# Kernel tuning notes

Hardware: AMD Instinct MI355X
Metric: run time of the kernel (lower is better)

The kernel has to match this reference:

```python
import jax, jax.numpy as jnp
import numpy as np

B, S, T, E, H = 2, 2048, 2048, 1024, 16
HD = E // H  # head_dim = 64


def setup_inputs() -> dict:
    key = jax.random.key(0)
    ks = jax.random.split(key, 12)
    sc = 1.0 / np.sqrt(E)
    inp = {
        "query": jax.random.normal(ks[0], (B, S, E), jnp.float32),
        "key": jax.random.normal(ks[1], (B, T, E), jnp.float32),
        "value": jax.random.normal(ks[2], (B, T, E), jnp.float32),
        "attn_mask": jnp.ones((S, T), jnp.int32),
        # nn.Linear params: y = x @ W.T + b
        "Wq": jax.random.normal(ks[3], (E, E), jnp.float32) * sc,
        "bq": jax.random.normal(ks[4], (E,), jnp.float32) * sc,
        "Wk": jax.random.normal(ks[5], (E, E), jnp.float32) * sc,
        "bk": jax.random.normal(ks[6], (E,), jnp.float32) * sc,
        "Wv": jax.random.normal(ks[7], (E, E), jnp.float32) * sc,
        "bv": jax.random.normal(ks[8], (E,), jnp.float32) * sc,
        "Wo": jax.random.normal(ks[9], (E, E), jnp.float32) * sc,
        "bo": jax.random.normal(ks[10], (E,), jnp.float32) * sc,
    }
    return inp


def reference(query, key, value, attn_mask, Wq, bq, Wk, bk, Wv, bv, Wo, bo):
    N, Sq, Ed = query.shape
    Tk = key.shape[1]
    # projections (torch Linear: x @ W.T + b)
    q = query @ Wq.T + bq
    k = key @ Wk.T + bk
    v = value @ Wv.T + bv
    # split heads -> (N, H, S, HD)
    q = q.reshape(N, Sq, H, HD).transpose(0, 2, 1, 3)
    k = k.reshape(N, Tk, H, HD).transpose(0, 2, 1, 3)
    v = v.reshape(N, Tk, H, HD).transpose(0, 2, 1, 3)
    # scaled dot-product scores: (N, H, S, T)
    energy = jnp.einsum("nhsd,nhtd->nhst", q, k) / jnp.sqrt(jnp.float32(HD))
    energy = jnp.where(attn_mask[None, None, :, :] == 0, -jnp.inf, energy)
    attn = jax.nn.softmax(energy, axis=3)
    # dropout is identity in eval mode
    out = jnp.einsum("nhst,nhtd->nshd", attn, v).reshape(N, Sq, Ed)
    return out @ Wo.T + bo
```

## Files before the change

kernel.cpp:

```cpp
#include <hip/hip_runtime.h>

typedef __attribute__((ext_vector_type(8))) short short8;
typedef __attribute__((ext_vector_type(4))) float f32x4;
typedef __attribute__((ext_vector_type(16))) float f32x16;

#define DEV __device__ __forceinline__

constexpr int Bb = 2, Ss = 2048, Tt = 2048, Ee = 1024, Hh = 16, HDd = 64;
constexpr int Mm = Bb * Ss;
constexpr size_t NX = (size_t)Mm * Ee;
constexpr size_t NW = (size_t)Ee * Ee;

constexpr size_t OFF_XQ   = 0;
constexpr size_t OFF_XK   = OFF_XQ + NX * 2;
constexpr size_t OFF_XV   = OFF_XK + NX * 2;
constexpr size_t OFF_WQ   = OFF_XV + NX * 2;
constexpr size_t OFF_WK   = OFF_WQ + NW * 2;
constexpr size_t OFF_WV   = OFF_WK + NW * 2;
constexpr size_t OFF_WO   = OFF_WV + NW * 2;
constexpr size_t OFF_QH   = OFF_WO + NW * 2;
constexpr size_t OFF_KH   = OFF_QH + NX * 2;
constexpr size_t OFF_VH   = OFF_KH + NX * 2;
constexpr size_t OFF_OB   = OFF_VH + NX * 2;
constexpr size_t OFF_FLAG = OFF_OB + NX * 2;

DEV unsigned short f2bf(float f) {
  union { float f; unsigned u; } v; v.f = f;
  unsigned r = v.u + 0x7fffu + ((v.u >> 16) & 1u);
  return (unsigned short)(r >> 16);
}

#define GLDS16(g, l) __builtin_amdgcn_global_load_lds(                         \
    (const __attribute__((address_space(1))) void*)(g),                        \
    (__attribute__((address_space(3))) void*)(l), 16, 0, 0)

#define PLSWAP(a, b) asm("v_permlane32_swap_b32 %0, %1" : "+v"(a), "+v"(b))
#define CVTPK(d, lo, hi_) asm("v_cvt_pk_bf16_f32 %0, %1, %2" : "=v"(d) : "v"(lo), "v"(hi_))

#if __has_builtin(__builtin_amdgcn_exp2f)
#define EXP2(x) __builtin_amdgcn_exp2f(x)
#else
#define EXP2(x) exp2f(x)
#endif

__global__ __launch_bounds__(256) void prep_kernel(
    const float* __restrict__ q, const float* __restrict__ k, const float* __restrict__ v,
    const float* __restrict__ wq, const float* __restrict__ wk,
    const float* __restrict__ wv, const float* __restrict__ wo,
    const int* __restrict__ mask,
    unsigned short* __restrict__ Xq, unsigned short* __restrict__ Xk, unsigned short* __restrict__ Xv,
    unsigned short* __restrict__ Wqb, unsigned short* __restrict__ Wkb,
    unsigned short* __restrict__ Wvb, unsigned short* __restrict__ Wob,
    int* __restrict__ flagZero)
{
  constexpr size_t NXv = NX / 4, NWv = NW / 4;
  constexpr size_t tot = 4 * NXv + 4 * NWv;
  for (size_t u = (size_t)blockIdx.x * blockDim.x + threadIdx.x; u < tot;
       u += (size_t)gridDim.x * blockDim.x) {
    if (u < 3 * NXv) {
      const float* src; unsigned short* dst; size_t off;
      if (u < NXv)            { src = q; dst = Xq; off = u; }
      else if (u < 2 * NXv)   { src = k; dst = Xk; off = u - NXv; }
      else                    { src = v; dst = Xv; off = u - 2 * NXv; }
      float4 f = ((const float4*)src)[off];
      ushort4 o; o.x = f2bf(f.x); o.y = f2bf(f.y); o.z = f2bf(f.z); o.w = f2bf(f.w);
      ((ushort4*)dst)[off] = o;
    } else if (u < 3 * NXv + 4 * NWv) {
      size_t uu = u - 3 * NXv;
      int wsel = (int)(uu / NWv); size_t off = uu % NWv;
      const float* src = wsel == 0 ? wq : wsel == 1 ? wk : wsel == 2 ? wv : wo;
      unsigned short* dst = wsel == 0 ? Wqb : wsel == 1 ? Wkb : wsel == 2 ? Wvb : Wob;
      float4 f = ((const float4*)src)[off];
      ushort4 o; o.x = f2bf(f.x); o.y = f2bf(f.y); o.z = f2bf(f.z); o.w = f2bf(f.w);
      ((ushort4*)dst)[off] = o;
    } else {
      size_t off = u - 3 * NXv - 4 * NWv;
      int4 m = ((const int4*)mask)[off];
      if (m.x == 0 || m.y == 0 || m.z == 0 || m.w == 0) *flagZero = 1;
    }
  }
}

DEV void gemm128(const unsigned short* __restrict__ A, const unsigned short* __restrict__ Bm,
                 unsigned short* Asm, unsigned short* Bsm, f32x4 acc[4][4], int K)
{
  const int t = threadIdx.x;
  const int w = t >> 6, lane = t & 63;
  const int l15 = lane & 15, l4 = lane >> 4;
  const int wm = w >> 1, wn = w & 1;
  const int srow = lane >> 2;
  const int skc  = (lane & 3) * 8;
#pragma unroll
  for (int mi = 0; mi < 4; ++mi)
#pragma unroll
    for (int ni = 0; ni < 4; ++ni) acc[mi][ni] = (f32x4){0.f, 0.f, 0.f, 0.f};

  for (int k0 = 0; k0 < K; k0 += 32) {
    GLDS16(A  + (size_t)(w * 16 + srow) * K + k0 + skc,        Asm + w * 512);
    GLDS16(A  + (size_t)(64 + w * 16 + srow) * K + k0 + skc,   Asm + 2048 + w * 512);
    GLDS16(Bm + (size_t)(w * 16 + srow) * K + k0 + skc,        Bsm + w * 512);
    GLDS16(Bm + (size_t)(64 + w * 16 + srow) * K + k0 + skc,   Bsm + 2048 + w * 512);
    __syncthreads();
    short8 af[4], bf[4];
#pragma unroll
    for (int mi = 0; mi < 4; ++mi)
      af[mi] = *(const short8*)&Asm[(wm * 64 + mi * 16 + l15) * 32 + l4 * 8];
#pragma unroll
    for (int ni = 0; ni < 4; ++ni)
      bf[ni] = *(const short8*)&Bsm[(wn * 64 + ni * 16 + l15) * 32 + l4 * 8];
#pragma unroll
    for (int mi = 0; mi < 4; ++mi)
#pragma unroll
      for (int ni = 0; ni < 4; ++ni)
        acc[mi][ni] = __builtin_amdgcn_mfma_f32_16x16x32_bf16(af[mi], bf[ni], acc[mi][ni], 0, 0, 0);
    __syncthreads();
  }
}

__global__ __launch_bounds__(256) void gemm_qkv(
    const unsigned short* __restrict__ Xq, const unsigned short* __restrict__ Xk,
    const unsigned short* __restrict__ Xv,
    const unsigned short* __restrict__ Wqb, const unsigned short* __restrict__ Wkb,
    const unsigned short* __restrict__ Wvb,
    const float* __restrict__ bq, const float* __restrict__ bk, const float* __restrict__ bv,
    unsigned short* __restrict__ Qh, unsigned short* __restrict__ Kh, unsigned short* __restrict__ Vh)
{
  __shared__ unsigned short Asm[128 * 32], Bsm[128 * 32];
  const int z = blockIdx.z;
  const unsigned short* A  = (z == 0) ? Xq  : (z == 1) ? Xk  : Xv;
  const unsigned short* Bw = (z == 0) ? Wqb : (z == 1) ? Wkb : Wvb;
  const float* bias        = (z == 0) ? bq  : (z == 1) ? bk  : bv;
  unsigned short* Out      = (z == 0) ? Qh  : (z == 1) ? Kh  : Vh;
  const int by = blockIdx.y, bx = blockIdx.x;
  f32x4 acc[4][4];
  gemm128(A + (size_t)by * 128 * Ee, Bw + (size_t)bx * 128 * Ee, Asm, Bsm, acc, Ee);
  const int t = threadIdx.x, w = t >> 6, lane = t & 63, l15 = lane & 15, l4 = lane >> 4;
  const int wm = w >> 1, wn = w & 1;
#pragma unroll
  for (int ni = 0; ni < 4; ++ni) {
    int col = bx * 128 + wn * 64 + ni * 16 + l15;
    float bcol = bias[col];
    int h = col >> 6, hd = col & 63;
#pragma unroll
    for (int mi = 0; mi < 4; ++mi) {
#pragma unroll
      for (int r = 0; r < 4; ++r) {
        int row = by * 128 + wm * 64 + mi * 16 + l4 * 4 + r;
        int b = row >> 11, s = row & 2047;
        Out[(((size_t)(b * Hh + h)) * Ss + s) * HDd + hd] = f2bf(acc[mi][ni][r] + bcol);
      }
    }
  }
}

__global__ __launch_bounds__(256) void gemm_out(
    const unsigned short* __restrict__ Ob, const unsigned short* __restrict__ Wob,
    const float* __restrict__ bo, float* __restrict__ out)
{
  __shared__ unsigned short Asm[128 * 32], Bsm[128 * 32];
  const int by = blockIdx.y, bx = blockIdx.x;
  f32x4 acc[4][4];
  gemm128(Ob + (size_t)by * 128 * Ee, Wob + (size_t)bx * 128 * Ee, Asm, Bsm, acc, Ee);
  const int t = threadIdx.x, w = t >> 6, lane = t & 63, l15 = lane & 15, l4 = lane >> 4;
  const int wm = w >> 1, wn = w & 1;
#pragma unroll
  for (int ni = 0; ni < 4; ++ni) {
    int col = bx * 128 + wn * 64 + ni * 16 + l15;
    float bcol = bo[col];
#pragma unroll
    for (int mi = 0; mi < 4; ++mi) {
#pragma unroll
      for (int r = 0; r < 4; ++r) {
        int row = by * 128 + wm * 64 + mi * 16 + l4 * 4 + r;
        out[(size_t)row * Ee + col] = acc[mi][ni][r] + bcol;
      }
    }
  }
}

__global__ __launch_bounds__(256) void attn_kernel(
    const unsigned short* __restrict__ Qh, const unsigned short* __restrict__ Kh,
    const unsigned short* __restrict__ Vh, const int* __restrict__ mask,
    const int* __restrict__ flagZero, unsigned short* __restrict__ Ob)
{
  __shared__ unsigned short Ks[2][64 * 64];
  __shared__ unsigned short Vt[2][64 * 72];
  const int bh = blockIdx.y, qt = blockIdx.x;
  const int tid = threadIdx.x, w = tid >> 6, lane = tid & 63;
  const int l31 = lane & 31, hi = lane >> 5;
  const bool useMask = (*flagZero != 0);
  const size_t bhBase = (size_t)bh * Ss * HDd;
  const int s0 = qt * 128 + w * 32;
  const float SCL = 0.18033688f;

  short8 qf[4];
#pragma unroll
  for (int ks = 0; ks < 4; ++ks)
    qf[ks] = *(const short8*)&Qh[bhBase + (size_t)(s0 + l31) * 64 + ks * 16 + hi * 8];

  f32x16 o0, o1;
#pragma unroll
  for (int r = 0; r < 16; ++r) { o0[r] = 0.f; o1[r] = 0.f; }
  float m_r = -1e30f, l_r = 0.f;

  const int kc0 = tid, kc1 = tid + 256;
  const int kr0 = kc0 >> 3, kg0 = (kc0 & 7) ^ (kr0 & 7);
  const int kr1 = kc1 >> 3, kg1 = (kc1 & 7) ^ (kr1 & 7);

  GLDS16(Kh + bhBase + (size_t)kr0 * 64 + kg0 * 8, &Ks[0][0] + w * 512);
  GLDS16(Kh + bhBase + (size_t)kr1 * 64 + kg1 * 8, &Ks[0][0] + 2048 + w * 512);
  {
    const unsigned short* vs = Vh + bhBase + (size_t)lane * 64 + w * 16;
    short8 v0 = *(const short8*)vs, v1 = *(const short8*)(vs + 8);
#pragma unroll
    for (int k2 = 0; k2 < 8; ++k2) Vt[0][(w * 16 + k2) * 72 + lane] = (unsigned short)v0[k2];
#pragma unroll
    for (int k2 = 0; k2 < 8; ++k2) Vt[0][(w * 16 + 8 + k2) * 72 + lane] = (unsigned short)v1[k2];
  }
  __syncthreads();

  int cur = 0;
  for (int kt = 0; kt < Tt; kt += 64) {
    const bool last = (kt + 64 >= Tt);
    short8 v0, v1;
    if (!last) {
      GLDS16(Kh + bhBase + (size_t)(kt + 64 + kr0) * 64 + kg0 * 8, &Ks[cur ^ 1][0] + w * 512);
      GLDS16(Kh + bhBase + (size_t)(kt + 64 + kr1) * 64 + kg1 * 8, &Ks[cur ^ 1][0] + 2048 + w * 512);
      const unsigned short* vs = Vh + bhBase + (size_t)(kt + 64 + lane) * 64 + w * 16;
      v0 = *(const short8*)vs; v1 = *(const short8*)(vs + 8);
    }

    f32x16 p0, p1;
#pragma unroll
    for (int r = 0; r < 16; ++r) { p0[r] = 0.f; p1[r] = 0.f; }
    const unsigned short* Kc = &Ks[cur][0];
#pragma unroll
    for (int ks = 0; ks < 4; ++ks) {
      int row0 = l31, row1 = 32 + l31;
      short8 ka0 = *(const short8*)&Kc[row0 * 64 + (((ks * 2 + hi) ^ (row0 & 7)) * 8)];
      short8 ka1 = *(const short8*)&Kc[row1 * 64 + (((ks * 2 + hi) ^ (row1 & 7)) * 8)];
      p0 = __builtin_amdgcn_mfma_f32_32x32x16_bf16(ka0, qf[ks], p0, 0, 0, 0);
      p1 = __builtin_amdgcn_mfma_f32_32x32x16_bf16(ka1, qf[ks], p1, 0, 0, 0);
    }

    if (useMask) {
      int sg = s0 + l31;
#pragma unroll
      for (int r = 0; r < 16; ++r) {
        int tg = kt + (r & 3) + 8 * (r >> 2) + 4 * hi;
        if (mask[(size_t)sg * Tt + tg] == 0)      p0[r] = -1e30f;
        if (mask[(size_t)sg * Tt + tg + 32] == 0) p1[r] = -1e30f;
      }
    }

    float pmax = p0[0];
#pragma unroll
    for (int r = 1; r < 16; ++r) pmax = fmaxf(pmax, p0[r]);
#pragma unroll
    for (int r = 0; r < 16; ++r) pmax = fmaxf(pmax, p1[r]);
    pmax = fmaxf(pmax, __shfl_xor(pmax, 32));

    if (!__all(pmax - m_r <= 44.0f)) {
      float mnew = fmaxf(m_r, pmax);
      float alpha = EXP2((m_r - mnew) * SCL);
      l_r *= alpha;
#pragma unroll
      for (int r = 0; r < 16; ++r) {
        int sr = (r & 3) + 8 * (r >> 2) + 4 * hi;
        float ar = __shfl(alpha, sr);
        o0[r] *= ar; o1[r] *= ar;
      }
      m_r = mnew;
    }
    float mm = m_r * SCL;
    float ps = 0.f;
#pragma unroll
    for (int r = 0; r < 16; ++r) { p0[r] = EXP2(fmaf(p0[r], SCL, -mm)); ps += p0[r]; }
#pragma unroll
    for (int r = 0; r < 16; ++r) { p1[r] = EXP2(fmaf(p1[r], SCL, -mm)); ps += p1[r]; }
    l_r += ps + __shfl_xor(ps, 32);

    short8 pa[4];
#define PACKKS(ks, PV)                                                         \
    {                                                                          \
      unsigned a0, a1, b0, b1; const int bse = 8 * ((ks) & 1);                 \
      CVTPK(a0, PV[bse + 0], PV[bse + 1]);                                     \
      CVTPK(a1, PV[bse + 2], PV[bse + 3]);                                     \
      CVTPK(b0, PV[bse + 4], PV[bse + 5]);                                     \
      CVTPK(b1, PV[bse + 6], PV[bse + 7]);                                     \
      PLSWAP(a0, b0); PLSWAP(a1, b1);                                          \
      union { unsigned u[4]; short8 s; } cc;                                   \
      cc.u[0] = a0; cc.u[1] = a1; cc.u[2] = b0; cc.u[3] = b1;                  \
      pa[ks] = cc.s;                                                           \
    }
    PACKKS(0, p0) PACKKS(1, p0) PACKKS(2, p1) PACKKS(3, p1)
#undef PACKKS

    const unsigned short* Vc = &Vt[cur][0];
#pragma unroll
    for (int ks = 0; ks < 4; ++ks) {
      short8 vf0 = *(const short8*)&Vc[(l31) * 72 + ks * 16 + hi * 8];
      short8 vf1 = *(const short8*)&Vc[(32 + l31) * 72 + ks * 16 + hi * 8];
      o0 = __builtin_amdgcn_mfma_f32_32x32x16_bf16(pa[ks], vf0, o0, 0, 0, 0);
      o1 = __builtin_amdgcn_mfma_f32_32x32x16_bf16(pa[ks], vf1, o1, 0, 0, 0);
    }

    if (!last) {
#pragma unroll
      for (int k2 = 0; k2 < 8; ++k2) Vt[cur ^ 1][(w * 16 + k2) * 72 + lane] = (unsigned short)v0[k2];
#pragma unroll
      for (int k2 = 0; k2 < 8; ++k2) Vt[cur ^ 1][(w * 16 + 8 + k2) * 72 + lane] = (unsigned short)v1[k2];
    }
    __syncthreads();
    cur ^= 1;
  }

  const int b = bh >> 4, h = bh & 15;
  float linv = l_r > 0.f ? 1.0f / l_r : 0.f;
#pragma unroll
  for (int r = 0; r < 16; ++r) {
    int sr = (r & 3) + 8 * (r >> 2) + 4 * hi;
    float li = __shfl(linv, sr);
    size_t rowbase = (size_t)(b * Ss + s0 + sr) * Ee + h * 64;
    Ob[rowbase + l31]      = f2bf(o0[r] * li);
    Ob[rowbase + 32 + l31] = f2bf(o1[r] * li);
  }
}

extern "C" void kernel_launch(void* const* d_in, const int* in_sizes, int n_in,
                              void* d_out, int out_size, void* d_ws, size_t ws_size,
                              hipStream_t stream) {
  const float* q   = (const float*)d_in[0];
  const float* k   = (const float*)d_in[1];
  const float* v   = (const float*)d_in[2];
  const int*  msk  = (const int*)d_in[3];
  const float* Wq  = (const float*)d_in[4];
  const float* bq  = (const float*)d_in[5];
  const float* Wk  = (const float*)d_in[6];
  const float* bk  = (const float*)d_in[7];
  const float* Wv  = (const float*)d_in[8];
  const float* bv  = (const float*)d_in[9];
  const float* Wo  = (const float*)d_in[10];
  const float* bo  = (const float*)d_in[11];
  float* out = (float*)d_out;

  char* ws = (char*)d_ws;
  unsigned short* Xq  = (unsigned short*)(ws + OFF_XQ);
  unsigned short* Xk  = (unsigned short*)(ws + OFF_XK);
  unsigned short* Xv  = (unsigned short*)(ws + OFF_XV);
  unsigned short* Wqb = (unsigned short*)(ws + OFF_WQ);
  unsigned short* Wkb = (unsigned short*)(ws + OFF_WK);
  unsigned short* Wvb = (unsigned short*)(ws + OFF_WV);
  unsigned short* Wob = (unsigned short*)(ws + OFF_WO);
  unsigned short* Qh  = (unsigned short*)(ws + OFF_QH);
  unsigned short* Kh  = (unsigned short*)(ws + OFF_KH);
  unsigned short* Vh  = (unsigned short*)(ws + OFF_VH);
  unsigned short* Ob  = (unsigned short*)(ws + OFF_OB);
  int* flagZero       = (int*)(ws + OFF_FLAG);

  hipMemsetAsync(flagZero, 0, 4, stream);
  prep_kernel<<<4096, 256, 0, stream>>>(q, k, v, Wq, Wk, Wv, Wo, msk,
                                        Xq, Xk, Xv, Wqb, Wkb, Wvb, Wob, flagZero);
  gemm_qkv<<<dim3(8, 32, 3), 256, 0, stream>>>(Xq, Xk, Xv, Wqb, Wkb, Wvb,
                                               bq, bk, bv, Qh, Kh, Vh);
  attn_kernel<<<dim3(16, 32), 256, 0, stream>>>(Qh, Kh, Vh, msk, flagZero, Ob);
  gemm_out<<<dim3(8, 32), 256, 0, stream>>>(Ob, Wob, bo, out);
}
```

Measured before the change: 151.6 us.

## Split attention KV range across wave pairs and merge partial softmax in LDS

Each block now covers 64 query rows instead of 128, and two waves share each 32-row group while handling alternate 64-key tiles of every 128-key chunk. The partial (m, l, O) states are merged through shared memory at the end. The grid doubles to 1024 blocks with a launch-bounds occupancy hint, and setprio is placed around the MFMA sections. The max and sum reductions are also rewritten as trees. In exchange, the software double-buffered prefetch is dropped: loads now happen synchronously each iteration with two barriers, which may expose memory latency, and the final merge adds LDS traffic.

```diff
diff --git a/kernel.cpp b/kernel.cpp
--- a/kernel.cpp
+++ b/kernel.cpp
@@ -178,7 +178,7 @@
   }
 }
 
-__global__ __launch_bounds__(256) void attn_kernel(
+__global__ __launch_bounds__(256, 4) void attn_kernel(
     const unsigned short* __restrict__ Qh, const unsigned short* __restrict__ Kh,
     const unsigned short* __restrict__ Vh, const int* __restrict__ mask,
     const int* __restrict__ flagZero, unsigned short* __restrict__ Ob)
@@ -188,9 +188,10 @@
   const int bh = blockIdx.y, qt = blockIdx.x;
   const int tid = threadIdx.x, w = tid >> 6, lane = tid & 63;
   const int l31 = lane & 31, hi = lane >> 5;
+  const int g = w >> 1, p = w & 1;
   const bool useMask = (*flagZero != 0);
   const size_t bhBase = (size_t)bh * Ss * HDd;
-  const int s0 = qt * 128 + w * 32;
+  const int s0 = qt * 64 + g * 32;
   const float SCL = 0.18033688f;
 
   short8 qf[4];
@@ -203,37 +204,36 @@
   for (int r = 0; r < 16; ++r) { o0[r] = 0.f; o1[r] = 0.f; }
   float m_r = -1e30f, l_r = 0.f;
 
-  const int kc0 = tid, kc1 = tid + 256;
-  const int kr0 = kc0 >> 3, kg0 = (kc0 & 7) ^ (kr0 & 7);
-  const int kr1 = kc1 >> 3, kg1 = (kc1 & 7) ^ (kr1 & 7);
-
-  GLDS16(Kh + bhBase + (size_t)kr0 * 64 + kg0 * 8, &Ks[0][0] + w * 512);
-  GLDS16(Kh + bhBase + (size_t)kr1 * 64 + kg1 * 8, &Ks[0][0] + 2048 + w * 512);
-  {
-    const unsigned short* vs = Vh + bhBase + (size_t)lane * 64 + w * 16;
-    short8 v0 = *(const short8*)vs, v1 = *(const short8*)(vs + 8);
-#pragma unroll
-    for (int k2 = 0; k2 < 8; ++k2) Vt[0][(w * 16 + k2) * 72 + lane] = (unsigned short)v0[k2];
-#pragma unroll
-    for (int k2 = 0; k2 < 8; ++k2) Vt[0][(w * 16 + 8 + k2) * 72 + lane] = (unsigned short)v1[k2];
-  }
-  __syncthreads();
-
-  int cur = 0;
-  for (int kt = 0; kt < Tt; kt += 64) {
-    const bool last = (kt + 64 >= Tt);
-    short8 v0, v1;
-    if (!last) {
-      GLDS16(Kh + bhBase + (size_t)(kt + 64 + kr0) * 64 + kg0 * 8, &Ks[cur ^ 1][0] + w * 512);
-      GLDS16(Kh + bhBase + (size_t)(kt + 64 + kr1) * 64 + kg1 * 8, &Ks[cur ^ 1][0] + 2048 + w * 512);
-      const unsigned short* vs = Vh + bhBase + (size_t)(kt + 64 + lane) * 64 + w * 16;
-      v0 = *(const short8*)vs; v1 = *(const short8*)(vs + 8);
-    }
-
+  const int kr0 = tid >> 3,        kg0 = (tid & 7) ^ (kr0 & 7);
+  const int kc1 = tid + 256;
+  const int kr1 = kc1 >> 3,        kg1 = (kc1 & 7) ^ (kr1 & 7);
+
+  const int myKt0 = p * 64;
+
+  for (int kt2 = 0; kt2 < Tt; kt2 += 128) {
+    const unsigned short* va = Vh + bhBase + (size_t)(kt2 + lane) * 64 + w * 16;
+    const unsigned short* vb = va + 64 * 64;
+    short8 va0 = *(const short8*)va, va1 = *(const short8*)(va + 8);
+    short8 vb0 = *(const short8*)vb, vb1 = *(const short8*)(vb + 8);
+    GLDS16(Kh + bhBase + (size_t)(kt2 + kr0) * 64 + kg0 * 8,       &Ks[0][0] + w * 512);
+    GLDS16(Kh + bhBase + (size_t)(kt2 + kr1) * 64 + kg1 * 8,       &Ks[0][0] + 2048 + w * 512);
+    GLDS16(Kh + bhBase + (size_t)(kt2 + 64 + kr0) * 64 + kg0 * 8,  &Ks[1][0] + w * 512);
+    GLDS16(Kh + bhBase + (size_t)(kt2 + 64 + kr1) * 64 + kg1 * 8,  &Ks[1][0] + 2048 + w * 512);
+#pragma unroll
+    for (int k2 = 0; k2 < 8; ++k2) {
+      Vt[0][(w * 16 + k2) * 72 + lane]     = (unsigned short)va0[k2];
+      Vt[0][(w * 16 + 8 + k2) * 72 + lane] = (unsigned short)va1[k2];
+      Vt[1][(w * 16 + k2) * 72 + lane]     = (unsigned short)vb0[k2];
+      Vt[1][(w * 16 + 8 + k2) * 72 + lane] = (unsigned short)vb1[k2];
+    }
+    __syncthreads();
+
+    const int kt = kt2 + myKt0;
     f32x16 p0, p1;
 #pragma unroll
     for (int r = 0; r < 16; ++r) { p0[r] = 0.f; p1[r] = 0.f; }
-    const unsigned short* Kc = &Ks[cur][0];
+    const unsigned short* Kc = &Ks[p][0];
+    __builtin_amdgcn_s_setprio(1);
 #pragma unroll
     for (int ks = 0; ks < 4; ++ks) {
       int row0 = l31, row1 = 32 + l31;
@@ -242,6 +242,7 @@
       p0 = __builtin_amdgcn_mfma_f32_32x32x16_bf16(ka0, qf[ks], p0, 0, 0, 0);
       p1 = __builtin_amdgcn_mfma_f32_32x32x16_bf16(ka1, qf[ks], p1, 0, 0, 0);
     }
+    __builtin_amdgcn_s_setprio(0);
 
     if (useMask) {
       int sg = s0 + l31;
@@ -253,11 +254,13 @@
       }
     }
 
-    float pmax = p0[0];
-#pragma unroll
-    for (int r = 1; r < 16; ++r) pmax = fmaxf(pmax, p0[r]);
-#pragma unroll
-    for (int r = 0; r < 16; ++r) pmax = fmaxf(pmax, p1[r]);
+    float mx[8];
+#pragma unroll
+    for (int i = 0; i < 8; ++i)
+      mx[i] = fmaxf(fmaxf(p0[2 * i], p0[2 * i + 1]), fmaxf(p1[2 * i], p1[2 * i + 1]));
+    mx[0] = fmaxf(mx[0], mx[4]); mx[1] = fmaxf(mx[1], mx[5]);
+    mx[2] = fmaxf(mx[2], mx[6]); mx[3] = fmaxf(mx[3], mx[7]);
+    float pmax = fmaxf(fmaxf(mx[0], mx[2]), fmaxf(mx[1], mx[3]));
     pmax = fmaxf(pmax, __shfl_xor(pmax, 32));
 
     if (!__all(pmax - m_r <= 44.0f)) {
@@ -273,11 +276,16 @@
       m_r = mnew;
     }
     float mm = m_r * SCL;
-    float ps = 0.f;
-#pragma unroll
-    for (int r = 0; r < 16; ++r) { p0[r] = EXP2(fmaf(p0[r], SCL, -mm)); ps += p0[r]; }
-#pragma unroll
-    for (int r = 0; r < 16; ++r) { p1[r] = EXP2(fmaf(p1[r], SCL, -mm)); ps += p1[r]; }
+#pragma unroll
+    for (int r = 0; r < 16; ++r) { p0[r] = EXP2(fmaf(p0[r], SCL, -mm)); }
+#pragma unroll
+    for (int r = 0; r < 16; ++r) { p1[r] = EXP2(fmaf(p1[r], SCL, -mm)); }
+    float sm[8];
+#pragma unroll
+    for (int i = 0; i < 8; ++i)
+      sm[i] = (p0[2 * i] + p0[2 * i + 1]) + (p1[2 * i] + p1[2 * i + 1]);
+    sm[0] += sm[4]; sm[1] += sm[5]; sm[2] += sm[6]; sm[3] += sm[7];
+    float ps = (sm[0] + sm[2]) + (sm[1] + sm[3]);
     l_r += ps + __shfl_xor(ps, 32);
 
     short8 pa[4];
@@ -296,7 +304,8 @@
     PACKKS(0, p0) PACKKS(1, p0) PACKKS(2, p1) PACKKS(3, p1)
 #undef PACKKS
 
-    const unsigned short* Vc = &Vt[cur][0];
+    const unsigned short* Vc = &Vt[p][0];
+    __builtin_amdgcn_s_setprio(1);
 #pragma unroll
     for (int ks = 0; ks < 4; ++ks) {
       short8 vf0 = *(const short8*)&Vc[(l31) * 72 + ks * 16 + hi * 8];
@@ -304,26 +313,40 @@
       o0 = __builtin_amdgcn_mfma_f32_32x32x16_bf16(pa[ks], vf0, o0, 0, 0, 0);
       o1 = __builtin_amdgcn_mfma_f32_32x32x16_bf16(pa[ks], vf1, o1, 0, 0, 0);
     }
-
-    if (!last) {
-#pragma unroll
-      for (int k2 = 0; k2 < 8; ++k2) Vt[cur ^ 1][(w * 16 + k2) * 72 + lane] = (unsigned short)v0[k2];
-#pragma unroll
-      for (int k2 = 0; k2 < 8; ++k2) Vt[cur ^ 1][(w * 16 + 8 + k2) * 72 + lane] = (unsigned short)v1[k2];
-    }
+    __builtin_amdgcn_s_setprio(0);
     __syncthreads();
-    cur ^= 1;
-  }
-
-  const int b = bh >> 4, h = bh & 15;
-  float linv = l_r > 0.f ? 1.0f / l_r : 0.f;
-#pragma unroll
-  for (int r = 0; r < 16; ++r) {
-    int sr = (r & 3) + 8 * (r >> 2) + 4 * hi;
-    float li = __shfl(linv, sr);
-    size_t rowbase = (size_t)(b * Ss + s0 + sr) * Ee + h * 64;
-    Ob[rowbase + l31]      = f2bf(o0[r] * li);
-    Ob[rowbase + 32 + l31] = f2bf(o1[r] * li);
+  }
+
+  float* Ox = (float*)&Ks[0][0];
+  float* Ml = (float*)&Vt[0][0];
+  if (p == 1) {
+#pragma unroll
+    for (int r = 0; r < 16; ++r) {
+      int sr = (r & 3) + 8 * (r >> 2) + 4 * hi;
+      Ox[g * 2048 + sr * 64 + l31]      = o0[r];
+      Ox[g * 2048 + sr * 64 + 32 + l31] = o1[r];
+    }
+    if (hi == 0) { Ml[g * 64 + l31] = m_r; Ml[g * 64 + 32 + l31] = l_r; }
+  }
+  __syncthreads();
+  if (p == 0) {
+    const int b = bh >> 4, h = bh & 15;
+    float m1v = Ml[g * 64 + l31], l1v = Ml[g * 64 + 32 + l31];
+    float mmF = fmaxf(m_r, m1v);
+    float f0 = EXP2((m_r - mmF) * SCL);
+    float f1 = EXP2((m1v - mmF) * SCL);
+    float lt = l_r * f0 + l1v * f1;
+    float linv = lt > 0.f ? 1.0f / lt : 0.f;
+    float s0f = f0 * linv, s1f = f1 * linv;
+#pragma unroll
+    for (int r = 0; r < 16; ++r) {
+      int sr = (r & 3) + 8 * (r >> 2) + 4 * hi;
+      float a = __shfl(s0f, sr);
+      float bb = __shfl(s1f, sr);
+      size_t rowbase = (size_t)(b * Ss + s0 + sr) * Ee + h * 64;
+      Ob[rowbase + l31]      = f2bf(o0[r] * a + Ox[g * 2048 + sr * 64 + l31] * bb);
+      Ob[rowbase + 32 + l31] = f2bf(o1[r] * a + Ox[g * 2048 + sr * 64 + 32 + l31] * bb);
+    }
   }
 }
 
@@ -363,6 +386,6 @@
                                         Xq, Xk, Xv, Wqb, Wkb, Wvb, Wob, flagZero);
   gemm_qkv<<<dim3(8, 32, 3), 256, 0, stream>>>(Xq, Xk, Xv, Wqb, Wkb, Wvb,
                                                bq, bk, bv, Qh, Kh, Vh);
-  attn_kernel<<<dim3(16, 32), 256, 0, stream>>>(Qh, Kh, Vh, msk, flagZero, Ob);
+  attn_kernel<<<dim3(32, 32), 256, 0, stream>>>(Qh, Kh, Vh, msk, flagZero, Ob);
   gemm_out<<<dim3(8, 32), 256, 0, stream>>>(Ob, Wob, bo, out);
 }
```

Result: no change. 152.3 us (+0.5%).
